# Kernel optimization log

Measured on AMD Instinct MI355X. Metric: run time of the kernel, lower is better.

Reference implementation:

```python
import jax, jax.numpy as jnp
import numpy as np

D_MODEL = 768
N_HEADS = 12
D_HEAD = D_MODEL // N_HEADS


def setup_inputs() -> dict:
    key = jax.random.key(0)
    k1, k2, k3 = jax.random.split(key, 3)
    B, N = 32, 1024
    x = jax.random.normal(k1, (B, N, D_MODEL), dtype=jnp.float32)
    w_qkv = jax.random.normal(k2, (D_MODEL, 3 * D_MODEL), dtype=jnp.float32) * (D_MODEL ** -0.5)
    b_qkv = jnp.zeros((3 * D_MODEL,), dtype=jnp.float32)
    w_proj = jax.random.normal(k3, (D_MODEL, D_MODEL), dtype=jnp.float32) * (D_MODEL ** -0.5)
    b_proj = jnp.zeros((D_MODEL,), dtype=jnp.float32)
    return {"x": x, "w_qkv": w_qkv, "b_qkv": b_qkv, "w_proj": w_proj, "b_proj": b_proj}


def reference(x, w_qkv, b_qkv, w_proj, b_proj):
    B, N, C = x.shape
    H, Dh = N_HEADS, D_HEAD
    # qkv projection: (B,N,3C) -> (3,B,H,N,Dh)
    qkv = (x @ w_qkv + b_qkv).reshape(B, N, 3, H, Dh).transpose(2, 0, 3, 1, 4)
    q, k, v = qkv[0], qkv[1], qkv[2]
    scale = Dh ** -0.5
    attn = jnp.einsum('bhnd,bhmd->bhnm', q, k) * scale  # (B,H,N,N)
    attn = jax.nn.softmax(attn, axis=-1)
    out = jnp.einsum('bhnm,bhmd->bhnd', attn, v)  # (B,H,N,Dh)
    out = out.transpose(0, 2, 1, 3).reshape(B, N, C)
    return out @ w_proj + b_proj
```

## Files before the change

kernel.cpp:

```cpp
#include <hip/hip_runtime.h>
#include <hip/hip_bf16.h>
#include <math.h>

#define BQ   32
#define SEQ  1024
#define DM   768
#define NH   12
#define DH   64
#define CQKV 2304
#define MROWS (BQ * SEQ)

#define QSCALE 0.1803368801f

typedef __attribute__((ext_vector_type(8))) short  short8;
typedef __attribute__((ext_vector_type(4))) short  short4v;
typedef __attribute__((ext_vector_type(4))) float  floatx4;

using bf16 = __hip_bfloat16;

#define G2L(g, l) __builtin_amdgcn_global_load_lds(                              \
        (const __attribute__((address_space(1))) void*)(g),                      \
        (__attribute__((address_space(3))) void*)(l), 16, 0, 0)

#define WAVE_SYNC() __builtin_amdgcn_wave_barrier()
#define MFMA16(a, b, c) __builtin_amdgcn_mfma_f32_16x16x32_bf16((a), (b), (c), 0, 0, 0)

__global__ void cast_f32_bf16(const float* __restrict__ in, bf16* __restrict__ out,
                              int n4)
{
    int idx = blockIdx.x * blockDim.x + threadIdx.x;
    if (idx < n4) {
        float4 v = ((const float4*)in)[idx];
        bf16 o[4] = { __float2bfloat16(v.x), __float2bfloat16(v.y),
                      __float2bfloat16(v.z), __float2bfloat16(v.w) };
        ((ushort4*)out)[idx] = *(const ushort4*)o;
    }
}

__global__ void transpose_cast(const float* __restrict__ in, bf16* __restrict__ out,
                               int R, int C)
{
    int idx = blockIdx.x * blockDim.x + threadIdx.x;
    if (idx < R * C) {
        int r = idx / C, c = idx % C;
        out[(size_t)c * R + r] = __float2bfloat16(in[idx]);
    }
}

__device__ __forceinline__ void gemm_mainloop(
    const bf16* __restrict__ X, const bf16* __restrict__ WT,
    int m0, int n0, int t, int w, int lr, int lq,
    bf16* As, bf16* Bs, floatx4 acc[4][4])
{
    const int wm = (w >> 1) * 64, wn = (w & 1) * 64;
    const bf16* gA = X  + (size_t)(m0 + (t >> 2)) * DM + (t & 3) * 8;
    const bf16* gB = WT + (size_t)(n0 + (t >> 2)) * DM + (t & 3) * 8;
    bf16* lA = As + w * 512;
    bf16* lB = Bs + w * 512;

    for (int k0 = 0; k0 < DM; k0 += 32) {
        G2L(gA + k0,           lA);
        G2L(gA + 64 * DM + k0, lA + 2048);
        G2L(gB + k0,           lB);
        G2L(gB + 64 * DM + k0, lB + 2048);
        __syncthreads();
        short8 af[4], bfr[4];
        #pragma unroll
        for (int at = 0; at < 4; ++at)
            af[at] = *(const short8*)(As + (wm + at * 16 + lr) * 32 + lq * 8);
        #pragma unroll
        for (int bt = 0; bt < 4; ++bt)
            bfr[bt] = *(const short8*)(Bs + (wn + bt * 16 + lr) * 32 + lq * 8);
        #pragma unroll
        for (int at = 0; at < 4; ++at)
            #pragma unroll
            for (int bt = 0; bt < 4; ++bt)
                acc[at][bt] = MFMA16(af[at], bfr[bt], acc[at][bt]);
        __syncthreads();
    }
}

__global__ __launch_bounds__(256) void gemm_qkv(
    const bf16* __restrict__ X, const bf16* __restrict__ WT,
    const float* __restrict__ bias,
    bf16* __restrict__ Qo, bf16* __restrict__ Ko, bf16* __restrict__ Vt)
{
    __shared__ __align__(16) bf16 As[4096], Bs[4096];
    const int t = threadIdx.x, w = t >> 6, lane = t & 63;
    const int lr = lane & 15, lq = lane >> 4;
    const int m0 = blockIdx.x * 128, n0 = blockIdx.y * 128;

    floatx4 acc[4][4] = {};
    gemm_mainloop(X, WT, m0, n0, t, w, lr, lq, As, Bs, acc);

    const int wm = (w >> 1) * 64, wn = (w & 1) * 64;
    const int cb = n0 + wn;
    const int which = cb / DM;
    const int hb    = (cb % DM) / DH;
    const float qmul = (which == 0) ? QSCALE : 1.0f;
    #pragma unroll
    for (int bt = 0; bt < 4; ++bt) {
        const int d = bt * 16 + lr;
        const float bv = bias[cb + bt * 16 + lr];
        #pragma unroll
        for (int at = 0; at < 4; ++at) {
            const int nb = m0 + wm + at * 16 + lq * 4;
            const int bb = nb >> 10, n = nb & (SEQ - 1);
            const size_t head = (size_t)bb * NH + hb;
            if (which == 2) {
                bf16 pk[4];
                #pragma unroll
                for (int rr = 0; rr < 4; ++rr)
                    pk[rr] = __float2bfloat16(acc[at][bt][rr] + bv);
                *(short4v*)(Vt + (head * DH + d) * SEQ + n) = *(const short4v*)pk;
            } else {
                bf16* base = (which ? Ko : Qo) + (head * SEQ + n) * DH + d;
                #pragma unroll
                for (int rr = 0; rr < 4; ++rr)
                    base[(size_t)rr * DH] = __float2bfloat16((acc[at][bt][rr] + bv) * qmul);
            }
        }
    }
}

__global__ __launch_bounds__(256) void gemm_proj(
    const bf16* __restrict__ A, const bf16* __restrict__ WT,
    const float* __restrict__ bias, float* __restrict__ out)
{
    __shared__ __align__(16) bf16 As[4096], Bs[4096];
    const int t = threadIdx.x, w = t >> 6, lane = t & 63;
    const int lr = lane & 15, lq = lane >> 4;
    const int m0 = blockIdx.x * 128, n0 = blockIdx.y * 128;

    floatx4 acc[4][4] = {};
    gemm_mainloop(A, WT, m0, n0, t, w, lr, lq, As, Bs, acc);

    const int wm = (w >> 1) * 64, wn = (w & 1) * 64;
    #pragma unroll
    for (int bt = 0; bt < 4; ++bt) {
        const float bv = bias[n0 + wn + bt * 16 + lr];
        #pragma unroll
        for (int at = 0; at < 4; ++at) {
            const int rg = m0 + wm + at * 16 + lq * 4;
            #pragma unroll
            for (int rr = 0; rr < 4; ++rr)
                out[(size_t)(rg + rr) * DM + n0 + wn + bt * 16 + lr] =
                    acc[at][bt][rr] + bv;
        }
    }
}

__global__ __launch_bounds__(256) void flash_attn(
    const bf16* __restrict__ Q, const bf16* __restrict__ K,
    const bf16* __restrict__ Vt, bf16* __restrict__ O)
{
    __shared__ __align__(16) bf16 Ks[2][2][64][32];
    __shared__ __align__(16) bf16 Vs[2][2][64][32];
    __shared__ __align__(16) bf16 Plds[4][32][72];
    const int w = threadIdx.x >> 6, lane = threadIdx.x & 63;
    const int lr = lane & 15, lq = lane >> 4;

    const int fid = blockIdx.x;
    const int g   = (fid & 7) + ((fid >> 6) << 3);
    const int x   = (fid >> 3) & 7;
    const int h   = g % NH, b = g / NH;
    const int qb  = x * 128 + w * 32;

    const bf16* Qh = Q  + (size_t)(b * NH + h) * SEQ * DH;
    const bf16* Kh = K  + (size_t)(b * NH + h) * SEQ * DH;
    const bf16* Vh = Vt + (size_t)(b * NH + h) * DH * SEQ;

    short8 bq[2][2];
    #pragma unroll
    for (int qs = 0; qs < 2; ++qs) {
        bq[qs][0] = *(const short8*)(Qh + (size_t)(qb + qs * 16 + lr) * DH + lq * 8);
        bq[qs][1] = *(const short8*)(Qh + (size_t)(qb + qs * 16 + lr) * DH + 32 + lq * 8);
    }

    floatx4 acc[2][4] = {};
    float li[2] = { 0.f, 0.f };

    const int srow = lane >> 2;
    const int ssw  = ((lane & 3) ^ ((lane >> 3) & 3)) * 8;
    const int rsw  = (lr >> 1) & 3;

    auto stage = [&](int bi, int jj) {
        #pragma unroll
        for (int i = 0; i < 4; ++i) {
            const int idx = w * 4 + i;
            if (idx < 8) {
                const int hh = idx >> 2, gg = idx & 3;
                G2L(Kh + (size_t)(jj + gg * 16 + srow) * DH + hh * 32 + ssw,
                    &Ks[bi][hh][gg * 16][0]);
            } else {
                const int vv = idx - 8, hh = vv >> 2, gg = vv & 3;
                G2L(Vh + (size_t)(gg * 16 + srow) * SEQ + jj + hh * 32 + ssw,
                    &Vs[bi][hh][gg * 16][0]);
            }
        }
    };

    stage(0, 0);
    __syncthreads();

    int cur = 0;
    for (int j0 = 0; j0 < SEQ; j0 += 64) {
        if (j0 + 64 < SEQ) stage(cur ^ 1, j0 + 64);

        short8 ak[4][2];
        #pragma unroll
        for (int jt = 0; jt < 4; ++jt) {
            ak[jt][0] = *(const short8*)(&Ks[cur][0][jt * 16 + lr][(lq ^ rsw) * 8]);
            ak[jt][1] = *(const short8*)(&Ks[cur][1][jt * 16 + lr][(lq ^ rsw) * 8]);
        }
        #pragma unroll
        for (int qs = 0; qs < 2; ++qs) {
            #pragma unroll
            for (int jt = 0; jt < 4; ++jt) {
                floatx4 c = {};
                c = MFMA16(ak[jt][0], bq[qs][0], c);
                c = MFMA16(ak[jt][1], bq[qs][1], c);
                bf16 pk[4];
                #pragma unroll
                for (int r = 0; r < 4; ++r) {
                    float p = exp2f(c[r]);
                    li[qs] += p;
                    pk[r] = __float2bfloat16(p);
                }
                *(short4v*)(&Plds[w][qs * 16 + lr][jt * 16 + lq * 4]) =
                    *(const short4v*)pk;
            }
        }
        WAVE_SYNC();

        short8 bv[4][2];
        #pragma unroll
        for (int dt = 0; dt < 4; ++dt) {
            bv[dt][0] = *(const short8*)(&Vs[cur][0][dt * 16 + lr][(lq ^ rsw) * 8]);
            bv[dt][1] = *(const short8*)(&Vs[cur][1][dt * 16 + lr][(lq ^ rsw) * 8]);
        }
        __builtin_amdgcn_s_setprio(1);
        #pragma unroll
        for (int qs = 0; qs < 2; ++qs) {
            short8 ap0 = *(const short8*)(&Plds[w][qs * 16 + lr][lq * 8]);
            short8 ap1 = *(const short8*)(&Plds[w][qs * 16 + lr][32 + lq * 8]);
            #pragma unroll
            for (int dt = 0; dt < 4; ++dt) {
                acc[qs][dt] = MFMA16(ap0, bv[dt][0], acc[qs][dt]);
                acc[qs][dt] = MFMA16(ap1, bv[dt][1], acc[qs][dt]);
            }
        }
        __builtin_amdgcn_s_setprio(0);

        __syncthreads();
        cur ^= 1;
    }

    #pragma unroll
    for (int qs = 0; qs < 2; ++qs) {
        li[qs] += __shfl_xor(li[qs], 16);
        li[qs] += __shfl_xor(li[qs], 32);
    }
    #pragma unroll
    for (int qs = 0; qs < 2; ++qs) {
        float inv[4];
        #pragma unroll
        for (int r = 0; r < 4; ++r)
            inv[r] = 1.f / __shfl(li[qs], lq * 4 + r);
        #pragma unroll
        for (int dt = 0; dt < 4; ++dt)
            #pragma unroll
            for (int r = 0; r < 4; ++r) {
                const int qi = qb + qs * 16 + lq * 4 + r;
                O[((size_t)b * SEQ + qi) * DM + h * DH + dt * 16 + lr] =
                    __float2bfloat16(acc[qs][dt][r] * inv[r]);
            }
    }
}

extern "C" void kernel_launch(void* const* d_in, const int* in_sizes, int n_in,
                              void* d_out, int out_size, void* d_ws, size_t ws_size,
                              hipStream_t stream)
{
    const float* x      = (const float*)d_in[0];
    const float* w_qkv  = (const float*)d_in[1];
    const float* b_qkv  = (const float*)d_in[2];
    const float* w_proj = (const float*)d_in[3];
    const float* b_proj = (const float*)d_in[4];
    float* out = (float*)d_out;

    bf16* ws = (bf16*)d_ws;
    size_t off = 0;
    bf16* wqkvT  = ws + off; off += (size_t)CQKV * DM;
    bf16* wprojT = ws + off; off += (size_t)DM * DM;
    bf16* Xb  = ws + off; off += (size_t)MROWS * DM;
    bf16* Qb  = ws + off; off += (size_t)BQ * NH * SEQ * DH;
    bf16* Kb  = ws + off; off += (size_t)BQ * NH * SEQ * DH;
    bf16* Vtb = ws + off; off += (size_t)BQ * NH * DH * SEQ;
    bf16* Ob  = ws + off; off += (size_t)MROWS * DM;

    cast_f32_bf16<<<(MROWS * DM / 4 + 255) / 256, 256, 0, stream>>>(x, Xb, MROWS * DM / 4);
    transpose_cast<<<(DM * CQKV + 255) / 256, 256, 0, stream>>>(w_qkv, wqkvT, DM, CQKV);
    transpose_cast<<<(DM * DM + 255) / 256, 256, 0, stream>>>(w_proj, wprojT, DM, DM);
    gemm_qkv<<<dim3(MROWS / 128, CQKV / 128), 256, 0, stream>>>(Xb, wqkvT, b_qkv, Qb, Kb, Vtb);
    flash_attn<<<dim3(BQ * NH * (SEQ / 128)), 256, 0, stream>>>(Qb, Kb, Vtb, Ob);
    gemm_proj<<<dim3(MROWS / 128, DM / 128), 256, 0, stream>>>(Ob, wprojT, b_proj, out);
}
```

Measured before the change: 588.8 us.

## Stage QKV epilogue through LDS for vector stores and remap blocks per XCD

The QKV GEMM epilogue now writes each wave's output tile into a padded per-wave LDS buffer, then issues 16-byte coalesced stores for Q/K rows and for transposed V rows, replacing scattered 2-byte and 8-byte global writes. Both GEMMs switch to a 1D grid whose block index is remapped so that consecutive blocks on the same XCD share M rows, with the aim of improving L2 reuse of the A operand. This adds LDS usage and wave-level syncs to the epilogue, and the remap hard-codes the grid sizes.

```diff
diff --git a/kernel.cpp b/kernel.cpp
--- a/kernel.cpp
+++ b/kernel.cpp
@@ -86,9 +86,13 @@
     bf16* __restrict__ Qo, bf16* __restrict__ Ko, bf16* __restrict__ Vt)
 {
     __shared__ __align__(16) bf16 As[4096], Bs[4096];
+    __shared__ __align__(16) bf16 Es[4][32][72];
     const int t = threadIdx.x, w = t >> 6, lane = t & 63;
     const int lr = lane & 15, lq = lane >> 4;
-    const int m0 = blockIdx.x * 128, n0 = blockIdx.y * 128;
+    const int id = blockIdx.x;
+    const int xcd = id & 7, o = id >> 3;
+    const int m0 = (xcd * 32 + o / 18) * 128;
+    const int n0 = (o % 18) * 128;
 
     floatx4 acc[4][4] = {};
     gemm_mainloop(X, WT, m0, n0, t, w, lr, lq, As, Bs, acc);
@@ -97,28 +101,59 @@
     const int cb = n0 + wn;
     const int which = cb / DM;
     const int hb    = (cb % DM) / DH;
+    const int nbw   = m0 + wm;
+    const int bb    = nbw >> 10, nloc = nbw & (SEQ - 1);
+    const size_t head = (size_t)bb * NH + hb;
     const float qmul = (which == 0) ? QSCALE : 1.0f;
-    #pragma unroll
-    for (int bt = 0; bt < 4; ++bt) {
-        const int d = bt * 16 + lr;
-        const float bv = bias[cb + bt * 16 + lr];
-        #pragma unroll
-        for (int at = 0; at < 4; ++at) {
-            const int nb = m0 + wm + at * 16 + lq * 4;
-            const int bb = nb >> 10, n = nb & (SEQ - 1);
-            const size_t head = (size_t)bb * NH + hb;
-            if (which == 2) {
-                bf16 pk[4];
+
+    if (which != 2) {
+        bf16* Out = (which ? Ko : Qo) + (head * SEQ + nloc) * DH;
+        #pragma unroll
+        for (int c2 = 0; c2 < 2; ++c2) {
+            #pragma unroll
+            for (int ah = 0; ah < 2; ++ah) {
+                const int at = c2 * 2 + ah;
                 #pragma unroll
-                for (int rr = 0; rr < 4; ++rr)
-                    pk[rr] = __float2bfloat16(acc[at][bt][rr] + bv);
-                *(short4v*)(Vt + (head * DH + d) * SEQ + n) = *(const short4v*)pk;
-            } else {
-                bf16* base = (which ? Ko : Qo) + (head * SEQ + n) * DH + d;
+                for (int bt = 0; bt < 4; ++bt) {
+                    const float bv = bias[cb + bt * 16 + lr];
+                    #pragma unroll
+                    for (int rr = 0; rr < 4; ++rr)
+                        Es[w][ah * 16 + lq * 4 + rr][bt * 16 + lr] =
+                            __float2bfloat16((acc[at][bt][rr] + bv) * qmul);
+                }
+            }
+            WAVE_SYNC();
+            #pragma unroll
+            for (int i = 0; i < 4; ++i) {
+                const int r = i * 8 + (lane >> 3), s = lane & 7;
+                short8 vv = *(const short8*)(&Es[w][r][s * 8]);
+                *(short8*)(Out + (size_t)(c2 * 32 + r) * DH + s * 8) = vv;
+            }
+            WAVE_SYNC();
+        }
+    } else {
+        bf16* Out = Vt + head * DH * SEQ + nloc;
+        #pragma unroll
+        for (int c2 = 0; c2 < 2; ++c2) {
+            #pragma unroll
+            for (int bh = 0; bh < 2; ++bh) {
+                const int bt = c2 * 2 + bh;
+                const float bv = bias[cb + bt * 16 + lr];
                 #pragma unroll
-                for (int rr = 0; rr < 4; ++rr)
-                    base[(size_t)rr * DH] = __float2bfloat16((acc[at][bt][rr] + bv) * qmul);
-            }
+                for (int at = 0; at < 4; ++at)
+                    #pragma unroll
+                    for (int rr = 0; rr < 4; ++rr)
+                        Es[w][bh * 16 + lr][at * 16 + lq * 4 + rr] =
+                            __float2bfloat16(acc[at][bt][rr] + bv);
+            }
+            WAVE_SYNC();
+            #pragma unroll
+            for (int i = 0; i < 4; ++i) {
+                const int r = i * 8 + (lane >> 3), s = lane & 7;
+                short8 vv = *(const short8*)(&Es[w][r][s * 8]);
+                *(short8*)(Out + (size_t)(c2 * 32 + r) * SEQ + s * 8) = vv;
+            }
+            WAVE_SYNC();
         }
     }
 }
@@ -130,7 +165,10 @@
     __shared__ __align__(16) bf16 As[4096], Bs[4096];
     const int t = threadIdx.x, w = t >> 6, lane = t & 63;
     const int lr = lane & 15, lq = lane >> 4;
-    const int m0 = blockIdx.x * 128, n0 = blockIdx.y * 128;
+    const int id = blockIdx.x;
+    const int xcd = id & 7, o = id >> 3;
+    const int m0 = (xcd * 32 + o / 6) * 128;
+    const int n0 = (o % 6) * 128;
 
     floatx4 acc[4][4] = {};
     gemm_mainloop(A, WT, m0, n0, t, w, lr, lq, As, Bs, acc);
@@ -302,7 +340,7 @@
     cast_f32_bf16<<<(MROWS * DM / 4 + 255) / 256, 256, 0, stream>>>(x, Xb, MROWS * DM / 4);
     transpose_cast<<<(DM * CQKV + 255) / 256, 256, 0, stream>>>(w_qkv, wqkvT, DM, CQKV);
     transpose_cast<<<(DM * DM + 255) / 256, 256, 0, stream>>>(w_proj, wprojT, DM, DM);
-    gemm_qkv<<<dim3(MROWS / 128, CQKV / 128), 256, 0, stream>>>(Xb, wqkvT, b_qkv, Qb, Kb, Vtb);
+    gemm_qkv<<<dim3(4608), 256, 0, stream>>>(Xb, wqkvT, b_qkv, Qb, Kb, Vtb);
     flash_attn<<<dim3(BQ * NH * (SEQ / 128)), 256, 0, stream>>>(Qb, Kb, Vtb, Ob);
-    gemm_proj<<<dim3(MROWS / 128, DM / 128), 256, 0, stream>>>(Ob, wprojT, b_proj, out);
-}
+    gemm_proj<<<dim3(1536), 256, 0, stream>>>(Ob, wprojT, b_proj, out);
+}
```

New measurement: 563.7 us. -4.3%, faster.
